# Kernel tuning notes

Hardware: AMD Instinct MI355X
Metric: run time of the kernel (lower is better)

The kernel has to match this reference:

```python
import jax, jax.numpy as jnp
import numpy as np

D_MODEL = 1024
N_HEADS = 16
D_K = D_MODEL // N_HEADS
THETA = 10000.0
BATCH = 1
SEQ = 4096


def setup_inputs() -> dict:
    key = jax.random.key(0)
    ks = jax.random.split(key, 5)
    std = (2.0 / (D_MODEL + D_MODEL)) ** 0.5
    mk = lambda k: jax.random.truncated_normal(k, -3.0, 3.0, (D_MODEL, D_MODEL), jnp.float32) * std
    return {
        "x": jax.random.normal(ks[0], (BATCH, SEQ, D_MODEL), jnp.float32),
        "Wq": mk(ks[1]),
        "Wk": mk(ks[2]),
        "Wv": mk(ks[3]),
        "Wo": mk(ks[4]),
    }


def _rope(x, pos, inv_freq):
    # x: [b, h, s, d_k]; pos: [s]; inv_freq: [d_k/2]
    angles = pos[:, None].astype(jnp.float32) * inv_freq  # [s, d_k/2]
    cos = jnp.repeat(jnp.cos(angles), 2, axis=-1)  # [s, d_k]
    sin = jnp.repeat(jnp.sin(angles), 2, axis=-1)
    # interleaved rotation: (-x1, x0, -x3, x2, ...)
    x_rot = jnp.stack([-x[..., 1::2], x[..., 0::2]], axis=-1).reshape(x.shape)
    return x * cos + x_rot * sin


def reference(x, Wq, Wk, Wv, Wo):
    b, s, _ = x.shape
    h, dk = N_HEADS, D_K
    proj = lambda W: jnp.einsum('bsi,oi->bso', x, W).reshape(b, s, h, dk).transpose(0, 2, 1, 3)
    q = proj(Wq)
    k = proj(Wk)
    v = proj(Wv)
    pos = jnp.arange(s)
    inv_freq = 1.0 / THETA ** (jnp.arange(0, dk, 2, dtype=jnp.float32) / dk)
    q = _rope(q, pos, inv_freq)
    k = _rope(k, pos, inv_freq)
    scores = jnp.einsum('bhqd,bhkd->bhqk', q, k) / jnp.sqrt(jnp.asarray(dk, jnp.float32))
    causal_mask = jnp.arange(s)[None, :] > jnp.arange(s)[:, None]  # [s, s], True above diag
    scores = jnp.where(causal_mask, -jnp.inf, scores)
    weights = jax.nn.softmax(scores, axis=-1)
    out = jnp.einsum('bhqk,bhkd->bhqd', weights, v)
    out = out.transpose(0, 2, 1, 3).reshape(b, s, h * dk)
    return jnp.einsum('bsi,oi->bso', out, Wo)
```

## Files before the change

### kernel.cpp

```cpp
#include <hip/hip_runtime.h>
#include <hip/hip_bf16.h>


typedef __hip_bfloat16 bf16;
using s16x4 = __attribute__((ext_vector_type(4))) short;
using s16x8 = __attribute__((ext_vector_type(8))) short;
using f32x4 = __attribute__((ext_vector_type(4))) float;

#define SEQ 4096
#define DMODEL 1024
#define NHEADS 16
#define DK 64
#define LOG2_THETA 13.287712379549449f
#define SCALE_LOG2E 0.1803368801111244f

#if defined(__has_builtin)
#if __has_builtin(__builtin_amdgcn_mfma_f32_16x16x16bf16_1k)
#define HAVE_MFMA16 1
#endif
#endif

__device__ __forceinline__ f32x4 mfma16(s16x4 a, s16x4 b, f32x4 c) {
#ifdef HAVE_MFMA16
  return __builtin_amdgcn_mfma_f32_16x16x16bf16_1k(a, b, c, 0, 0, 0);
#else
  asm volatile("v_mfma_f32_16x16x16_bf16 %0, %1, %2, %0"
               : "+v"(c) : "v"(a), "v"(b));
  return c;
#endif
}

__device__ __forceinline__ void async16(const bf16* g, bf16* l) {
  __builtin_amdgcn_global_load_lds(
      (const __attribute__((address_space(1))) unsigned int*)g,
      (__attribute__((address_space(3))) unsigned int*)l, 16, 0, 0);
}

__global__ __launch_bounds__(256)
void conv_kernel(const float* __restrict__ s0, const float* __restrict__ s1,
                 const float* __restrict__ s2, const float* __restrict__ s3,
                 const float* __restrict__ s4,
                 bf16* __restrict__ d0, bf16* __restrict__ d1,
                 bf16* __restrict__ d2, bf16* __restrict__ d3,
                 bf16* __restrict__ d4) {
  const int z = blockIdx.z;
  const float* s = (z == 0) ? s0 : (z == 1) ? s1 : (z == 2) ? s2 : (z == 3) ? s3 : s4;
  bf16* d = (z == 0) ? d0 : (z == 1) ? d1 : (z == 2) ? d2 : (z == 3) ? d3 : d4;
  const int n = (z == 0) ? SEQ * DMODEL : DMODEL * DMODEL;
  for (int i = (blockIdx.x * 256 + threadIdx.x) * 8; i < n; i += 512 * 256 * 8) {
    const float4 a = *(const float4*)(s + i);
    const float4 b = *(const float4*)(s + i + 4);
    union { bf16 h[8]; s16x8 v; } u;
    u.h[0] = __float2bfloat16(a.x); u.h[1] = __float2bfloat16(a.y);
    u.h[2] = __float2bfloat16(a.z); u.h[3] = __float2bfloat16(a.w);
    u.h[4] = __float2bfloat16(b.x); u.h[5] = __float2bfloat16(b.y);
    u.h[6] = __float2bfloat16(b.z); u.h[7] = __float2bfloat16(b.w);
    *(s16x8*)(d + i) = u.v;
  }
}

__global__ __launch_bounds__(256)
void gemm_kernel(const bf16* __restrict__ A,
                 const bf16* __restrict__ W0, const bf16* __restrict__ W1,
                 const bf16* __restrict__ W2,
                 bf16* __restrict__ D0, bf16* __restrict__ D1,
                 bf16* __restrict__ D2) {
  const int mode = (int)blockIdx.z;
  const bf16* __restrict__ W = (mode == 1) ? W1 : (mode == 2) ? W2 : W0;
  bf16* __restrict__ D = (mode == 1) ? D1 : (mode == 2) ? D2 : D0;

  const int tid  = threadIdx.x;
  const int lane = tid & 63;
  const int wave = tid >> 6;
  const int wm = wave >> 1, wn = wave & 1;
  const int quad = lane >> 4, l16 = lane & 15;
  const int m0 = blockIdx.x * 128;
  const int n0 = blockIdx.y * 128;

  __shared__ __align__(16) char gsm[49152];
  bf16* const smem = (bf16*)gsm;

  f32x4 acc[4][4] = {};

  const int ldrow = lane >> 2;
  const int ldcol = (lane & 3) * 8;

  auto stage = [&](int b, int k0) {
#pragma unroll
    for (int c = 0; c < 2; ++c) {
      const int chunk = wave * 2 + c;
      const int row = chunk * 16 + ldrow;
      async16(&A[(size_t)(m0 + row) * DMODEL + k0 + ldcol],
              &smem[b * 8192 + chunk * 512]);
      async16(&W[(size_t)(n0 + row) * DMODEL + k0 + ldcol],
              &smem[b * 8192 + 4096 + chunk * 512]);
    }
  };

  stage(0, 0);
  __syncthreads();

  for (int t = 0; t < 32; ++t) {
    const int cur = t & 1;
    if (t < 31) stage(cur ^ 1, (t + 1) * 32);

    s16x8 af[4], bfr[4];
#pragma unroll
    for (int i = 0; i < 4; ++i)
      af[i] = *(const s16x8*)&smem[cur * 8192 + (wm * 64 + i * 16 + l16) * 32 + quad * 8];
#pragma unroll
    for (int j = 0; j < 4; ++j)
      bfr[j] = *(const s16x8*)&smem[cur * 8192 + 4096 + (wn * 64 + j * 16 + l16) * 32 + quad * 8];
#pragma unroll
    for (int i = 0; i < 4; ++i)
#pragma unroll
      for (int j = 0; j < 4; ++j)
        acc[i][j] = __builtin_amdgcn_mfma_f32_16x16x32_bf16(af[i], bfr[j],
                                                            acc[i][j], 0, 0, 0);
    __syncthreads();
  }

  bf16* const Esw = (bf16*)(gsm + 16384) + wave * 4096;

  if (mode == 2) {
#pragma unroll
    for (int i = 0; i < 4; ++i)
#pragma unroll
      for (int j = 0; j < 4; ++j)
#pragma unroll
        for (int r = 0; r < 4; ++r)
          Esw[(j * 16 + l16) * 64 + i * 16 + quad * 4 + r] =
              __float2bfloat16(acc[i][j][r]);
  } else {
#pragma unroll
    for (int i = 0; i < 4; ++i)
#pragma unroll
      for (int j = 0; j < 4; ++j)
#pragma unroll
        for (int r = 0; r < 4; ++r)
          Esw[(i * 16 + quad * 4 + r) * 64 + j * 16 + l16] =
              __float2bfloat16(acc[i][j][r]);
  }
  __syncthreads();

  const int h = (n0 >> 6) + wn;
  const int g  = lane >> 3;
  const int c8 = (lane & 7) * 8;

  if (mode == 2) {
#pragma unroll
    for (int t = 0; t < 8; ++t) {
      const int d = t * 8 + g;
      const s16x8 v = *(const s16x8*)&Esw[d * 64 + c8];
      *(s16x8*)&D[((size_t)h * DK + d) * SEQ + m0 + wm * 64 + c8] = v;
    }
  } else {
    const float qs = (mode == 0) ? SCALE_LOG2E : 1.0f;
    float sn[4], cs[4], s8[4], c8r[4];
    const int srow0 = m0 + wm * 64 + g;
#pragma unroll
    for (int k = 0; k < 4; ++k) {
      const int p = (c8 >> 1) + k;
      const float invf = __builtin_amdgcn_exp2f((float)p * (-2.0f / 64.0f) * LOG2_THETA);
      sincosf((float)srow0 * invf, &sn[k], &cs[k]);
      sincosf(8.0f * invf, &s8[k], &c8r[k]);
      sn[k] *= qs; cs[k] *= qs;
    }
#pragma unroll
    for (int t = 0; t < 8; ++t) {
      const int rl = t * 8 + g;
      union { bf16 h[8]; s16x8 v; } u, o;
      u.v = *(const s16x8*)&Esw[rl * 64 + c8];
#pragma unroll
      for (int k = 0; k < 4; ++k) {
        const float x0 = __bfloat162float(u.h[2 * k]);
        const float x1 = __bfloat162float(u.h[2 * k + 1]);
        o.h[2 * k]     = __float2bfloat16(x0 * cs[k] - x1 * sn[k]);
        o.h[2 * k + 1] = __float2bfloat16(x1 * cs[k] + x0 * sn[k]);
        const float ns_ = sn[k] * c8r[k] + cs[k] * s8[k];
        cs[k] = cs[k] * c8r[k] - sn[k] * s8[k];
        sn[k] = ns_;
      }
      const int srow = m0 + wm * 64 + rl;
      *(s16x8*)&D[((size_t)h * SEQ + srow) * DK + c8] = o.v;
    }
  }
}

__global__ __launch_bounds__(256)
void gemmo_kernel(const bf16* __restrict__ A, const bf16* __restrict__ W,
                  float* __restrict__ Df) {
  const int tid  = threadIdx.x;
  const int lane = tid & 63;
  const int wave = tid >> 6;
  const int wm = wave >> 1, wn = wave & 1;
  const int quad = lane >> 4, l16 = lane & 15;
  const int m0 = blockIdx.x * 64;
  const int n0 = blockIdx.y * 64;

  __shared__ __align__(16) bf16 sm[2][4096];

  f32x4 acc[2][2] = {};
  const int ldrow = lane >> 2;
  const int ldcol = (lane & 3) * 8;

  auto stage = [&](int b, int k0) {
    const int row = wave * 16 + ldrow;
    async16(&A[(size_t)(m0 + row) * DMODEL + k0 + ldcol], &sm[b][wave * 512]);
    async16(&W[(size_t)(n0 + row) * DMODEL + k0 + ldcol],
            &sm[b][2048 + wave * 512]);
  };

  stage(0, 0);
  __syncthreads();

  for (int t = 0; t < 32; ++t) {
    const int cur = t & 1;
    if (t < 31) stage(cur ^ 1, (t + 1) * 32);

    s16x8 af[2], bfr[2];
#pragma unroll
    for (int i = 0; i < 2; ++i)
      af[i] = *(const s16x8*)&sm[cur][(wm * 32 + i * 16 + l16) * 32 + quad * 8];
#pragma unroll
    for (int j = 0; j < 2; ++j)
      bfr[j] = *(const s16x8*)&sm[cur][2048 + (wn * 32 + j * 16 + l16) * 32 + quad * 8];
#pragma unroll
    for (int i = 0; i < 2; ++i)
#pragma unroll
      for (int j = 0; j < 2; ++j)
        acc[i][j] = __builtin_amdgcn_mfma_f32_16x16x32_bf16(af[i], bfr[j],
                                                            acc[i][j], 0, 0, 0);
    __syncthreads();
  }

#pragma unroll
  for (int i = 0; i < 2; ++i)
#pragma unroll
    for (int j = 0; j < 2; ++j) {
      const int col = n0 + wn * 32 + j * 16 + l16;
#pragma unroll
      for (int r = 0; r < 4; ++r) {
        const int srow = m0 + wm * 32 + i * 16 + quad * 4 + r;
        Df[(size_t)srow * DMODEL + col] = acc[i][j][r];
      }
    }
}

__global__ __launch_bounds__(256, 4)
void attn_kernel(const bf16* __restrict__ Q, const bf16* __restrict__ K,
                 const bf16* __restrict__ Vt, bf16* __restrict__ O) {
  const int tid  = threadIdx.x;
  const int lane = tid & 63;
  const int wave = tid >> 6;
  const int quad = lane >> 4, l16 = lane & 15;
  const int wq = wave & 1;
  const int wk = wave >> 1;

  const int i  = (int)blockIdx.x;
  const int j  = i & 255;
  const int vv = 3 - (i >> 8);
  const int h  = j & 15;
  const int a  = j >> 4;
  const int qb = vv * 16 + ((vv & 1) ? (15 - a) : a);

  const bf16* __restrict__ Qh = Q + (size_t)h * SEQ * DK;
  const bf16* __restrict__ Kh = K + (size_t)h * SEQ * DK;
  const bf16* __restrict__ Vh = Vt + (size_t)h * DK * SEQ;

  __shared__ __align__(16) char smemb[32768];
  bf16* __restrict__ smem = (bf16*)smemb;
  bf16* __restrict__ KsB = smem;
  bf16* __restrict__ VsB = smem + 8192;

  const int srow = lane >> 3;
  const int schk = (lane & 7) ^ srow;
  const int xsw  = l16 & 7;

  const int q0 = qb * 64;
  const int qw = q0 + wq * 32;
  const int nb = qb + 1;

  const short ONE = 0x3F80;
  const s16x4 ones4 = {ONE, ONE, ONE, ONE};

  s16x8 aq[2][2];
#pragma unroll
  for (int gq = 0; gq < 2; ++gq) {
    const size_t qr = (size_t)(qw + gq * 16 + l16) * DK;
    aq[gq][0] = *(const s16x8*)&Qh[qr + quad * 8];
    aq[gq][1] = *(const s16x8*)&Qh[qr + 32 + quad * 8];
  }

  f32x4 oacc[2][4] = {};
  f32x4 lacc[2] = {};

  {
#pragma unroll
    for (int c = 0; c < 2; ++c) {
      const int chunk = wave * 2 + c;
      async16(Kh + (size_t)(chunk * 8 + srow) * 64 + schk * 8,
              &KsB[chunk * 512]);
      async16(Vh + (size_t)(chunk * 8 + srow) * SEQ + schk * 8,
              &VsB[chunk * 512]);
    }
  }
  __syncthreads();

  for (int kb = 0; kb < nb; ++kb) {
    const int cur = kb & 1;
    if (kb + 1 < nb) {
      const int nxt = cur ^ 1;
      const int kv1 = (kb + 1) * 64;
      const bf16* kg = Kh + (size_t)kv1 * DK;
#pragma unroll
      for (int c = 0; c < 2; ++c) {
        const int chunk = wave * 2 + c;
        async16(kg + (size_t)(chunk * 8 + srow) * 64 + schk * 8,
                &KsB[nxt * 4096 + chunk * 512]);
        async16(Vh + (size_t)(chunk * 8 + srow) * SEQ + kv1 + schk * 8,
                &VsB[nxt * 4096 + chunk * 512]);
      }
    }

    const bf16* __restrict__ Ksc = &KsB[cur * 4096];
    const bf16* __restrict__ Vsc = &VsB[cur * 4096];

    f32x4 sc[2][2] = {};
    __builtin_amdgcn_s_setprio(1);
#pragma unroll
    for (int hh = 0; hh < 2; ++hh) {
      const bf16* kr = &Ksc[(wk * 32 + hh * 16 + l16) * 64];
      const s16x8 ak0 = *(const s16x8*)&kr[(quad ^ xsw) * 8];
      const s16x8 ak1 = *(const s16x8*)&kr[((quad + 4) ^ xsw) * 8];
#pragma unroll
      for (int gq = 0; gq < 2; ++gq) {
        sc[gq][hh] = __builtin_amdgcn_mfma_f32_16x16x32_bf16(ak0, aq[gq][0], sc[gq][hh], 0, 0, 0);
        sc[gq][hh] = __builtin_amdgcn_mfma_f32_16x16x32_bf16(ak1, aq[gq][1], sc[gq][hh], 0, 0, 0);
      }
    }
    __builtin_amdgcn_s_setprio(0);

    if (kb == nb - 1) {
#pragma unroll
      for (int gq = 0; gq < 2; ++gq) {
        const int lim = wq * 32 + gq * 16 + l16 - wk * 32 - quad * 4;
#pragma unroll
        for (int hh = 0; hh < 2; ++hh)
#pragma unroll
          for (int r = 0; r < 4; ++r)
            if (hh * 16 + r > lim) sc[gq][hh][r] = -1e30f;
      }
    }

    s16x4 ap[2][2];
#pragma unroll
    for (int gq = 0; gq < 2; ++gq)
#pragma unroll
      for (int hh = 0; hh < 2; ++hh) {
        union { bf16 b[4]; s16x4 v; } pk;
#pragma unroll
        for (int r = 0; r < 4; ++r)
          pk.b[r] = __float2bfloat16(__builtin_amdgcn_exp2f(sc[gq][hh][r]));
        ap[gq][hh] = pk.v;
      }

    __builtin_amdgcn_s_setprio(1);
#pragma unroll
    for (int hh = 0; hh < 2; ++hh) {
      const int cg = wk * 4 + hh * 2 + (quad >> 1);
      const int eo = ((cg ^ xsw) << 3) + (quad & 1) * 4;
#pragma unroll
      for (int ns = 0; ns < 4; ++ns) {
        const s16x4 bv = *(const s16x4*)&Vsc[(ns * 16 + l16) * 64 + eo];
#pragma unroll
        for (int gq = 0; gq < 2; ++gq)
          oacc[gq][ns] = mfma16(ap[gq][hh], bv, oacc[gq][ns]);
      }
    }
#pragma unroll
    for (int gq = 0; gq < 2; ++gq)
#pragma unroll
      for (int hh = 0; hh < 2; ++hh)
        lacc[gq] = mfma16(ap[gq][hh], ones4, lacc[gq]);
    __builtin_amdgcn_s_setprio(0);

    __syncthreads();
  }

  float* __restrict__ Ored = (float*)smemb;
  float* __restrict__ lred = (float*)(smemb + 16896);
  bf16*  __restrict__ Obuf = (bf16*)(smemb + 17408);

  if (wk == 1) {
#pragma unroll
    for (int gq = 0; gq < 2; ++gq) {
#pragma unroll
      for (int ns = 0; ns < 4; ++ns)
#pragma unroll
        for (int r = 0; r < 4; ++r)
          Ored[(wq * 32 + gq * 16 + quad * 4 + r) * 66 + ns * 16 + l16] =
              oacc[gq][ns][r];
      if (l16 == 0)
#pragma unroll
        for (int r = 0; r < 4; ++r)
          lred[wq * 32 + gq * 16 + quad * 4 + r] = lacc[gq][r];
    }
  }
  __syncthreads();
  if (wk == 0) {
#pragma unroll
    for (int gq = 0; gq < 2; ++gq) {
      float rl[4];
#pragma unroll
      for (int r = 0; r < 4; ++r)
        rl[r] = __builtin_amdgcn_rcpf(lred[wq * 32 + gq * 16 + quad * 4 + r] +
                                      lacc[gq][r]);
#pragma unroll
      for (int ns = 0; ns < 4; ++ns)
#pragma unroll
        for (int r = 0; r < 4; ++r) {
          const int row = wq * 32 + gq * 16 + quad * 4 + r;
          const float val = oacc[gq][ns][r] + Ored[row * 66 + ns * 16 + l16];
          Obuf[row * 72 + ns * 16 + l16] = __float2bfloat16(val * rl[r]);
        }
    }
  }
  __syncthreads();
#pragma unroll
  for (int p = 0; p < 2; ++p) {
    const int row = p * 32 + (tid >> 3);
    const int c8 = (tid & 7) * 8;
    const s16x8 v = *(const s16x8*)&Obuf[row * 72 + c8];
    *(s16x8*)&O[(size_t)(q0 + row) * DMODEL + h * DK + c8] = v;
  }
}

extern "C" void kernel_launch(void* const* d_in, const int* in_sizes, int n_in,
                              void* d_out, int out_size, void* d_ws, size_t ws_size,
                              hipStream_t stream) {
  const float* x  = (const float*)d_in[0];
  const float* Wq = (const float*)d_in[1];
  const float* Wk = (const float*)d_in[2];
  const float* Wv = (const float*)d_in[3];
  const float* Wo = (const float*)d_in[4];
  float* out = (float*)d_out;

  bf16* ws = (bf16*)d_ws;
  bf16* xb   = ws;
  bf16* Wqb  = xb  + (size_t)SEQ * DMODEL;
  bf16* Wkb  = Wqb + (size_t)DMODEL * DMODEL;
  bf16* Wvb  = Wkb + (size_t)DMODEL * DMODEL;
  bf16* Wob  = Wvb + (size_t)DMODEL * DMODEL;
  bf16* Qb   = Wob + (size_t)DMODEL * DMODEL;
  bf16* Kb   = Qb  + (size_t)SEQ * DMODEL;
  bf16* Vtb  = Kb  + (size_t)SEQ * DMODEL;
  bf16* Attn = Vtb + (size_t)SEQ * DMODEL;

  conv_kernel<<<dim3(512, 1, 5), 256, 0, stream>>>(
      x, Wq, Wk, Wv, Wo, xb, Wqb, Wkb, Wvb, Wob);
  gemm_kernel<<<dim3(SEQ / 128, DMODEL / 128, 3), 256, 0, stream>>>(
      xb, Wqb, Wkb, Wvb, Qb, Kb, Vtb);
  attn_kernel<<<dim3(64 * NHEADS), 256, 0, stream>>>(Qb, Kb, Vtb, Attn);
  gemmo_kernel<<<dim3(SEQ / 64, DMODEL / 64), 256, 0, stream>>>(
      Attn, Wob, out);
}
```

Before: 190.6 us.

## Split attention key tile across four waves with 512-thread blocks

Doubles the attention kernel's block size from 4 to 8 waves. Each wave now handles 16 keys of every 64-key tile instead of 32, and each wave loads one K/V chunk instead of two. The per-wave partial outputs and row sums are combined through shared memory in three serialized steps. The goal is more waves in flight to hide latency, at the cost of extra reduction syncs and a tighter register budget under the new launch bounds.

```diff
diff --git a/kernel.cpp b/kernel.cpp
--- a/kernel.cpp
+++ b/kernel.cpp
@@ -247,7 +247,7 @@
     }
 }
 
-__global__ __launch_bounds__(256, 4)
+__global__ __launch_bounds__(512, 4)
 void attn_kernel(const bf16* __restrict__ Q, const bf16* __restrict__ K,
                  const bf16* __restrict__ Vt, bf16* __restrict__ O) {
   const int tid  = threadIdx.x;
@@ -295,16 +295,8 @@
   f32x4 oacc[2][4] = {};
   f32x4 lacc[2] = {};
 
-  {
-#pragma unroll
-    for (int c = 0; c < 2; ++c) {
-      const int chunk = wave * 2 + c;
-      async16(Kh + (size_t)(chunk * 8 + srow) * 64 + schk * 8,
-              &KsB[chunk * 512]);
-      async16(Vh + (size_t)(chunk * 8 + srow) * SEQ + schk * 8,
-              &VsB[chunk * 512]);
-    }
-  }
+  async16(Kh + (size_t)(wave * 8 + srow) * 64 + schk * 8, &KsB[wave * 512]);
+  async16(Vh + (size_t)(wave * 8 + srow) * SEQ + schk * 8, &VsB[wave * 512]);
   __syncthreads();
 
   for (int kb = 0; kb < nb; ++kb) {
@@ -312,31 +304,25 @@
     if (kb + 1 < nb) {
       const int nxt = cur ^ 1;
       const int kv1 = (kb + 1) * 64;
-      const bf16* kg = Kh + (size_t)kv1 * DK;
-#pragma unroll
-      for (int c = 0; c < 2; ++c) {
-        const int chunk = wave * 2 + c;
-        async16(kg + (size_t)(chunk * 8 + srow) * 64 + schk * 8,
-                &KsB[nxt * 4096 + chunk * 512]);
-        async16(Vh + (size_t)(chunk * 8 + srow) * SEQ + kv1 + schk * 8,
-                &VsB[nxt * 4096 + chunk * 512]);
-      }
+      async16(Kh + (size_t)kv1 * DK + (size_t)(wave * 8 + srow) * 64 + schk * 8,
+              &KsB[nxt * 4096 + wave * 512]);
+      async16(Vh + (size_t)(wave * 8 + srow) * SEQ + kv1 + schk * 8,
+              &VsB[nxt * 4096 + wave * 512]);
     }
 
     const bf16* __restrict__ Ksc = &KsB[cur * 4096];
     const bf16* __restrict__ Vsc = &VsB[cur * 4096];
 
-    f32x4 sc[2][2] = {};
+    f32x4 sc[2] = {};
     __builtin_amdgcn_s_setprio(1);
-#pragma unroll
-    for (int hh = 0; hh < 2; ++hh) {
-      const bf16* kr = &Ksc[(wk * 32 + hh * 16 + l16) * 64];
+    {
+      const bf16* kr = &Ksc[(wk * 16 + l16) * 64];
       const s16x8 ak0 = *(const s16x8*)&kr[(quad ^ xsw) * 8];
       const s16x8 ak1 = *(const s16x8*)&kr[((quad + 4) ^ xsw) * 8];
 #pragma unroll
       for (int gq = 0; gq < 2; ++gq) {
-        sc[gq][hh] = __builtin_amdgcn_mfma_f32_16x16x32_bf16(ak0, aq[gq][0], sc[gq][hh], 0, 0, 0);
-        sc[gq][hh] = __builtin_amdgcn_mfma_f32_16x16x32_bf16(ak1, aq[gq][1], sc[gq][hh], 0, 0, 0);
+        sc[gq] = __builtin_amdgcn_mfma_f32_16x16x32_bf16(ak0, aq[gq][0], sc[gq], 0, 0, 0);
+        sc[gq] = __builtin_amdgcn_mfma_f32_16x16x32_bf16(ak1, aq[gq][1], sc[gq], 0, 0, 0);
       }
     }
     __builtin_amdgcn_s_setprio(0);
@@ -344,45 +330,38 @@
     if (kb == nb - 1) {
 #pragma unroll
       for (int gq = 0; gq < 2; ++gq) {
-        const int lim = wq * 32 + gq * 16 + l16 - wk * 32 - quad * 4;
-#pragma unroll
-        for (int hh = 0; hh < 2; ++hh)
-#pragma unroll
-          for (int r = 0; r < 4; ++r)
-            if (hh * 16 + r > lim) sc[gq][hh][r] = -1e30f;
+        const int lim = wq * 32 + gq * 16 + l16 - wk * 16 - quad * 4;
+#pragma unroll
+        for (int r = 0; r < 4; ++r)
+          if (r > lim) sc[gq][r] = -1e30f;
       }
     }
 
-    s16x4 ap[2][2];
-#pragma unroll
-    for (int gq = 0; gq < 2; ++gq)
-#pragma unroll
-      for (int hh = 0; hh < 2; ++hh) {
-        union { bf16 b[4]; s16x4 v; } pk;
-#pragma unroll
-        for (int r = 0; r < 4; ++r)
-          pk.b[r] = __float2bfloat16(__builtin_amdgcn_exp2f(sc[gq][hh][r]));
-        ap[gq][hh] = pk.v;
-      }
+    s16x4 ap[2];
+#pragma unroll
+    for (int gq = 0; gq < 2; ++gq) {
+      union { bf16 b[4]; s16x4 v; } pk;
+#pragma unroll
+      for (int r = 0; r < 4; ++r)
+        pk.b[r] = __float2bfloat16(__builtin_amdgcn_exp2f(sc[gq][r]));
+      ap[gq] = pk.v;
+    }
 
     __builtin_amdgcn_s_setprio(1);
-#pragma unroll
-    for (int hh = 0; hh < 2; ++hh) {
-      const int cg = wk * 4 + hh * 2 + (quad >> 1);
+    {
+      const int cg = wk * 2 + (quad >> 1);
       const int eo = ((cg ^ xsw) << 3) + (quad & 1) * 4;
 #pragma unroll
       for (int ns = 0; ns < 4; ++ns) {
         const s16x4 bv = *(const s16x4*)&Vsc[(ns * 16 + l16) * 64 + eo];
 #pragma unroll
         for (int gq = 0; gq < 2; ++gq)
-          oacc[gq][ns] = mfma16(ap[gq][hh], bv, oacc[gq][ns]);
+          oacc[gq][ns] = mfma16(ap[gq], bv, oacc[gq][ns]);
       }
     }
 #pragma unroll
     for (int gq = 0; gq < 2; ++gq)
-#pragma unroll
-      for (int hh = 0; hh < 2; ++hh)
-        lacc[gq] = mfma16(ap[gq][hh], ones4, lacc[gq]);
+      lacc[gq] = mfma16(ap[gq], ones4, lacc[gq]);
     __builtin_amdgcn_s_setprio(0);
 
     __syncthreads();
@@ -392,7 +371,7 @@
   float* __restrict__ lred = (float*)(smemb + 16896);
   bf16*  __restrict__ Obuf = (bf16*)(smemb + 17408);
 
-  if (wk == 1) {
+  if (wk == 3) {
 #pragma unroll
     for (int gq = 0; gq < 2; ++gq) {
 #pragma unroll
@@ -405,6 +384,38 @@
 #pragma unroll
         for (int r = 0; r < 4; ++r)
           lred[wq * 32 + gq * 16 + quad * 4 + r] = lacc[gq][r];
+    }
+  }
+  __syncthreads();
+  if (wk == 2) {
+#pragma unroll
+    for (int gq = 0; gq < 2; ++gq) {
+#pragma unroll
+      for (int ns = 0; ns < 4; ++ns)
+#pragma unroll
+        for (int r = 0; r < 4; ++r)
+          Ored[(wq * 32 + gq * 16 + quad * 4 + r) * 66 + ns * 16 + l16] +=
+              oacc[gq][ns][r];
+      if (l16 == 0)
+#pragma unroll
+        for (int r = 0; r < 4; ++r)
+          lred[wq * 32 + gq * 16 + quad * 4 + r] += lacc[gq][r];
+    }
+  }
+  __syncthreads();
+  if (wk == 1) {
+#pragma unroll
+    for (int gq = 0; gq < 2; ++gq) {
+#pragma unroll
+      for (int ns = 0; ns < 4; ++ns)
+#pragma unroll
+        for (int r = 0; r < 4; ++r)
+          Ored[(wq * 32 + gq * 16 + quad * 4 + r) * 66 + ns * 16 + l16] +=
+              oacc[gq][ns][r];
+      if (l16 == 0)
+#pragma unroll
+        for (int r = 0; r < 4; ++r)
+          lred[wq * 32 + gq * 16 + quad * 4 + r] += lacc[gq][r];
     }
   }
   __syncthreads();
@@ -427,9 +438,8 @@
     }
   }
   __syncthreads();
-#pragma unroll
-  for (int p = 0; p < 2; ++p) {
-    const int row = p * 32 + (tid >> 3);
+  {
+    const int row = tid >> 3;
     const int c8 = (tid & 7) * 8;
     const s16x8 v = *(const s16x8*)&Obuf[row * 72 + c8];
     *(s16x8*)&O[(size_t)(q0 + row) * DMODEL + h * DK + c8] = v;
@@ -461,7 +471,7 @@
       x, Wq, Wk, Wv, Wo, xb, Wqb, Wkb, Wvb, Wob);
   gemm_kernel<<<dim3(SEQ / 128, DMODEL / 128, 3), 256, 0, stream>>>(
       xb, Wqb, Wkb, Wvb, Qb, Kb, Vtb);
-  attn_kernel<<<dim3(64 * NHEADS), 256, 0, stream>>>(Qb, Kb, Vtb, Attn);
+  attn_kernel<<<dim3(64 * NHEADS), 512, 0, stream>>>(Qb, Kb, Vtb, Attn);
   gemmo_kernel<<<dim3(SEQ / 64, DMODEL / 64), 256, 0, stream>>>(
       Attn, Wob, out);
 }
```

Measured after the change: 194.6 us. 1.02x slower.

## Split causal attention KV range across two blocks with atomic fp32 merge

Applied to the files above, without the earlier changes.

Each query tile's key/value range is split in half, and the two halves are handled by separate blocks, doubling the grid to 2048 blocks. Unnormalized partial outputs and row sums are accumulated with atomicAdd into a zeroed fp32 workspace. A new merge kernel then normalizes and writes the bf16 attention output. The aim is more parallelism and better load balance across the causal workload. The cost is a memset, fp32 atomic traffic and an extra kernel launch. This relies on the softmax not using a per-block running max, so the partials can be summed directly.

```diff
diff --git a/kernel.cpp b/kernel.cpp
--- a/kernel.cpp
+++ b/kernel.cpp
@@ -249,7 +249,8 @@
 
 __global__ __launch_bounds__(256, 4)
 void attn_kernel(const bf16* __restrict__ Q, const bf16* __restrict__ K,
-                 const bf16* __restrict__ Vt, bf16* __restrict__ O) {
+                 const bf16* __restrict__ Vt,
+                 float* __restrict__ Of, float* __restrict__ lf) {
   const int tid  = threadIdx.x;
   const int lane = tid & 63;
   const int wave = tid >> 6;
@@ -258,8 +259,10 @@
   const int wk = wave >> 1;
 
   const int i  = (int)blockIdx.x;
-  const int j  = i & 255;
-  const int vv = 3 - (i >> 8);
+  const int u  = i & 1023;
+  const int c  = 1 - (i >> 10);
+  const int j  = u & 255;
+  const int vv = 3 - (u >> 8);
   const int h  = j & 15;
   const int a  = j >> 4;
   const int qb = vv * 16 + ((vv & 1) ? (15 - a) : a);
@@ -280,6 +283,8 @@
   const int q0 = qb * 64;
   const int qw = q0 + wq * 32;
   const int nb = qb + 1;
+  const int k0 = c ? (nb >> 1) : 0;
+  const int k1 = c ? nb : (nb >> 1);
 
   const short ONE = 0x3F80;
   const s16x4 ones4 = {ONE, ONE, ONE, ONE};
@@ -296,26 +301,27 @@
   f32x4 lacc[2] = {};
 
   {
-#pragma unroll
-    for (int c = 0; c < 2; ++c) {
-      const int chunk = wave * 2 + c;
-      async16(Kh + (size_t)(chunk * 8 + srow) * 64 + schk * 8,
+    const bf16* kg = Kh + (size_t)k0 * 64 * DK;
+#pragma unroll
+    for (int cc = 0; cc < 2; ++cc) {
+      const int chunk = wave * 2 + cc;
+      async16(kg + (size_t)(chunk * 8 + srow) * 64 + schk * 8,
               &KsB[chunk * 512]);
-      async16(Vh + (size_t)(chunk * 8 + srow) * SEQ + schk * 8,
+      async16(Vh + (size_t)(chunk * 8 + srow) * SEQ + k0 * 64 + schk * 8,
               &VsB[chunk * 512]);
     }
   }
   __syncthreads();
 
-  for (int kb = 0; kb < nb; ++kb) {
-    const int cur = kb & 1;
-    if (kb + 1 < nb) {
+  for (int kb = k0; kb < k1; ++kb) {
+    const int cur = (kb - k0) & 1;
+    if (kb + 1 < k1) {
       const int nxt = cur ^ 1;
       const int kv1 = (kb + 1) * 64;
       const bf16* kg = Kh + (size_t)kv1 * DK;
 #pragma unroll
-      for (int c = 0; c < 2; ++c) {
-        const int chunk = wave * 2 + c;
+      for (int cc = 0; cc < 2; ++cc) {
+        const int chunk = wave * 2 + cc;
         async16(kg + (size_t)(chunk * 8 + srow) * 64 + schk * 8,
                 &KsB[nxt * 4096 + chunk * 512]);
         async16(Vh + (size_t)(chunk * 8 + srow) * SEQ + kv1 + schk * 8,
@@ -390,7 +396,6 @@
 
   float* __restrict__ Ored = (float*)smemb;
   float* __restrict__ lred = (float*)(smemb + 16896);
-  bf16*  __restrict__ Obuf = (bf16*)(smemb + 17408);
 
   if (wk == 1) {
 #pragma unroll
@@ -409,31 +414,46 @@
   }
   __syncthreads();
   if (wk == 0) {
+    float* __restrict__ Ot = Of + (size_t)(h * 64 + qb) * 4096;
+    float* __restrict__ lt = lf + (h * 64 + qb) * 64;
 #pragma unroll
     for (int gq = 0; gq < 2; ++gq) {
-      float rl[4];
-#pragma unroll
-      for (int r = 0; r < 4; ++r)
-        rl[r] = __builtin_amdgcn_rcpf(lred[wq * 32 + gq * 16 + quad * 4 + r] +
-                                      lacc[gq][r]);
 #pragma unroll
       for (int ns = 0; ns < 4; ++ns)
 #pragma unroll
         for (int r = 0; r < 4; ++r) {
           const int row = wq * 32 + gq * 16 + quad * 4 + r;
-          const float val = oacc[gq][ns][r] + Ored[row * 66 + ns * 16 + l16];
-          Obuf[row * 72 + ns * 16 + l16] = __float2bfloat16(val * rl[r]);
+          atomicAdd(&Ot[row * 64 + ns * 16 + l16],
+                    oacc[gq][ns][r] + Ored[row * 66 + ns * 16 + l16]);
         }
-    }
-  }
-  __syncthreads();
-#pragma unroll
-  for (int p = 0; p < 2; ++p) {
-    const int row = p * 32 + (tid >> 3);
-    const int c8 = (tid & 7) * 8;
-    const s16x8 v = *(const s16x8*)&Obuf[row * 72 + c8];
-    *(s16x8*)&O[(size_t)(q0 + row) * DMODEL + h * DK + c8] = v;
-  }
+      if (l16 == 0)
+#pragma unroll
+        for (int r = 0; r < 4; ++r) {
+          const int row = wq * 32 + gq * 16 + quad * 4 + r;
+          atomicAdd(&lt[row], lacc[gq][r] + lred[row]);
+        }
+    }
+  }
+}
+
+__global__ __launch_bounds__(256)
+void merge_kernel(const float* __restrict__ Of, const float* __restrict__ lf,
+                  bf16* __restrict__ Attn) {
+  const int t  = (int)blockIdx.x;
+  const int h  = t >> 6, qb = t & 63;
+  const int q0 = qb * 64;
+  const float* __restrict__ Ot = Of + (size_t)t * 4096;
+  const float* __restrict__ lt = lf + t * 64;
+  const int row = threadIdx.x >> 2;
+  const int c0  = (threadIdx.x & 3) * 16;
+  const float rl = __builtin_amdgcn_rcpf(lt[row]);
+  union { bf16 b[16]; s16x8 v[2]; } o;
+#pragma unroll
+  for (int k = 0; k < 16; ++k)
+    o.b[k] = __float2bfloat16(Ot[row * 64 + c0 + k] * rl);
+  bf16* dst = &Attn[(size_t)(q0 + row) * DMODEL + h * DK + c0];
+  *(s16x8*)dst = o.v[0];
+  *(s16x8*)(dst + 8) = o.v[1];
 }
 
 extern "C" void kernel_launch(void* const* d_in, const int* in_sizes, int n_in,
@@ -456,12 +476,18 @@
   bf16* Kb   = Qb  + (size_t)SEQ * DMODEL;
   bf16* Vtb  = Kb  + (size_t)SEQ * DMODEL;
   bf16* Attn = Vtb + (size_t)SEQ * DMODEL;
+  float* Of  = (float*)(Attn + (size_t)SEQ * DMODEL);
+  float* lf  = Of + (size_t)NHEADS * 64 * 4096;
+
+  hipMemsetAsync(Of, 0, (size_t)(NHEADS * 64 * 4096 + NHEADS * 64 * 64) * 4,
+                 stream);
 
   conv_kernel<<<dim3(512, 1, 5), 256, 0, stream>>>(
       x, Wq, Wk, Wv, Wo, xb, Wqb, Wkb, Wvb, Wob);
   gemm_kernel<<<dim3(SEQ / 128, DMODEL / 128, 3), 256, 0, stream>>>(
       xb, Wqb, Wkb, Wvb, Qb, Kb, Vtb);
-  attn_kernel<<<dim3(64 * NHEADS), 256, 0, stream>>>(Qb, Kb, Vtb, Attn);
+  attn_kernel<<<dim3(2048), 256, 0, stream>>>(Qb, Kb, Vtb, Of, lf);
+  merge_kernel<<<dim3(1024), 256, 0, stream>>>(Of, lf, Attn);
   gemmo_kernel<<<dim3(SEQ / 64, DMODEL / 64), 256, 0, stream>>>(
       Attn, Wob, out);
 }
```

New measurement: 204.5 us. +7.3%, slower.
